# Performance work log

Hardware: AMD Instinct MI355X
Metric: run time of the kernel (lower is better)

## Reference

```python
import jax, jax.numpy as jnp
import numpy as np

B, S, D = 4, 2048, 1024
H = 16
DH = D // H          # 64
DFF = 4096
EPS = 1e-5


def _layer_norm(x, gamma, beta):
    mu = jnp.mean(x, axis=-1, keepdims=True)
    var = jnp.mean(jnp.square(x - mu), axis=-1, keepdims=True)
    return (x - mu) * jax.lax.rsqrt(var + EPS) * gamma + beta


def setup_inputs() -> dict:
    key = jax.random.key(0)
    ks = jax.random.split(key, 8)
    s_in = 1.0 / np.sqrt(D)
    s_ff = 1.0 / np.sqrt(DFF)
    return {
        "x": jax.random.normal(ks[0], (B, S, D), dtype=jnp.float32),
        # per-head qkv weights stacked: [H, D, 3*DH] (nn.Linear, bias=False)
        "Wqkv": jax.random.normal(ks[1], (H, D, 3 * DH), dtype=jnp.float32) * s_in,
        "Wproj": jax.random.normal(ks[2], (D, D), dtype=jnp.float32) * s_in,
        "bproj": jnp.zeros((D,), dtype=jnp.float32),
        "ln1_g": jnp.ones((D,), dtype=jnp.float32),
        "ln1_b": jnp.zeros((D,), dtype=jnp.float32),
        "ln2_g": jnp.ones((D,), dtype=jnp.float32),
        "ln2_b": jnp.zeros((D,), dtype=jnp.float32),
        "W1": jax.random.normal(ks[3], (D, DFF), dtype=jnp.float32) * s_in,
        "b1": jnp.zeros((DFF,), dtype=jnp.float32),
        "W2": jax.random.normal(ks[4], (DFF, D), dtype=jnp.float32) * s_ff,
        "b2": jnp.zeros((D,), dtype=jnp.float32),
    }


def reference(x, Wqkv, Wproj, bproj, ln1_g, ln1_b, ln2_g, ln2_b, W1, b1, W2, b2):
    # fused multi-head QKV projection: [B,S,D] x [H,D,3*DH] -> [B,H,S,3*DH]
    qkv = jnp.einsum('bsd,hde->bhse', x, Wqkv)
    q, k, v = jnp.split(qkv, 3, axis=-1)          # each [B,H,S,DH]
    scale = 1.0 / jnp.sqrt(jnp.asarray(DH, dtype=x.dtype))
    scores = jnp.einsum('bhsd,bhtd->bhst', q, k) * scale   # [B,H,S,S]
    causal = jnp.tril(jnp.ones((S, S), dtype=bool))
    scores = jnp.where(causal, scores, jnp.finfo(x.dtype).min)
    attn = jax.nn.softmax(scores, axis=-1)
    heads = jnp.einsum('bhst,bhtd->bhsd', attn, v)          # [B,H,S,DH]
    att_out = heads.transpose(0, 2, 1, 3).reshape(B, S, D)  # concat heads
    att_out = att_out @ Wproj + bproj
    out = _layer_norm(x + att_out, ln1_g, ln1_b)            # dropout = identity (eval)
    mlp_out = (jax.nn.gelu(out @ W1 + b1, approximate=False)) @ W2 + b2
    out = _layer_norm(out + mlp_out, ln2_g, ln2_b)
    return out
```

## Files before the change

### kernel.cpp

```cpp
#include <hip/hip_runtime.h>
#include <math.h>

#define BB 4
#define SS 2048
#define DD 1024
#define HH 16
#define DHH 64
#define DFF 4096
static constexpr float LN_EPS = 1e-5f;

typedef __bf16 bf16x8 __attribute__((ext_vector_type(8)));
typedef float f32x4 __attribute__((ext_vector_type(4)));
typedef unsigned short u16x8 __attribute__((ext_vector_type(8)));

__device__ __forceinline__ unsigned short f2bf(float f) {
    return __builtin_bit_cast(unsigned short, (__bf16)f);
}

__device__ __forceinline__ float fexp2(float x) {
    return __builtin_amdgcn_exp2f(x);
}

__device__ __forceinline__ void gl_lds16(const unsigned short* g,
                                         unsigned short* l) {
    __builtin_amdgcn_global_load_lds(
        (const __attribute__((address_space(1))) unsigned int*)g,
        (__attribute__((address_space(3))) unsigned int*)l, 16, 0, 0);
}

#define GBAR()                               \
    do {                                     \
        asm volatile("" ::: "memory");       \
        __builtin_amdgcn_s_barrier();        \
        asm volatile("" ::: "memory");       \
    } while (0)
#define VMCNT(n) asm volatile("s_waitcnt vmcnt(" #n ")" ::: "memory")

__global__ __launch_bounds__(256) void transpose_bf16_kernel(
    const float* __restrict__ in, unsigned short* __restrict__ outT,
    int R, int C) {
    __shared__ float t[64][65];
    const int r0 = blockIdx.y * 64, c0 = blockIdx.x * 64;
    const int cl = threadIdx.x & 63, rl = threadIdx.x >> 6;
#pragma unroll
    for (int rr = 0; rr < 16; ++rr)
        t[rl + rr * 4][cl] = in[(size_t)(r0 + rl + rr * 4) * C + c0 + cl];
    __syncthreads();
#pragma unroll
    for (int rr = 0; rr < 16; ++rr)
        outT[(size_t)(c0 + rl + rr * 4) * R + r0 + cl] = f2bf(t[cl][rl + rr * 4]);
}

__global__ __launch_bounds__(256) void repack_wqkv_bf16_kernel(
    const float* __restrict__ Wqkv, unsigned short* __restrict__ Wq2T) {
    __shared__ float t[64][65];
    const int h = blockIdx.z;
    const int d0 = blockIdx.y * 64, e0 = blockIdx.x * 64;
    const int cl = threadIdx.x & 63, rl = threadIdx.x >> 6;
#pragma unroll
    for (int rr = 0; rr < 16; ++rr)
        t[rl + rr * 4][cl] =
            Wqkv[((size_t)h * DD + d0 + rl + rr * 4) * 192 + e0 + cl];
    __syncthreads();
#pragma unroll
    for (int rr = 0; rr < 16; ++rr)
        Wq2T[((size_t)h * 192 + e0 + rl + rr * 4) * DD + d0 + cl] =
            f2bf(t[cl][rl + rr * 4]);
}

__global__ __launch_bounds__(256) void f2bf_kernel(
    const float* __restrict__ in, unsigned short* __restrict__ out, int n) {
    int i = blockIdx.x * 256 + threadIdx.x;
    if (i < n) out[i] = f2bf(in[i]);
}

template <int RS>
__device__ __forceinline__ void stage_half(const unsigned short* __restrict__ G,
                                           int ldK, int growbase, int kbase,
                                           unsigned short* lbase, int tid) {
#pragma unroll
    for (int s = 0; s < 2; ++s) {
        const int c16 = s * 512 + tid;
        const int r = c16 >> 3, c = c16 & 7;
        const int grow =
            growbase + ((r >> RS) << (RS + 1)) + (r & ((1 << RS) - 1));
        const int gcol = kbase + ((c ^ (r & 7)) << 3);
        gl_lds16(&G[(size_t)grow * ldK + gcol], &lbase[c16 << 3]);
    }
}

__device__ __forceinline__ void stage_64(const unsigned short* __restrict__ G,
                                         int ldK, int growbase, int kbase,
                                         unsigned short* lbase, int tid) {
    const int r = tid >> 3, c = tid & 7;
    const int grow = growbase + ((r >> 5) << 6) + (r & 31);
    const int gcol = kbase + ((c ^ (r & 7)) << 3);
    gl_lds16(&G[(size_t)grow * ldK + gcol], &lbase[tid << 3]);
}

__device__ __forceinline__ void stage_kv8(const unsigned short* __restrict__ src,
                                          size_t rstride, unsigned short* dst,
                                          int tid) {
    const int r = tid >> 3, c = tid & 7;
    gl_lds16(&src[(size_t)r * rstride + ((c ^ (r & 7)) << 3)], &dst[tid << 3]);
}

__device__ __forceinline__ void read_afrag(const unsigned short* s, int base,
                                           int wm, int l15, int g,
                                           bf16x8 af[4][2]) {
#pragma unroll
    for (int ii = 0; ii < 4; ++ii) {
        const int lr = wm * 64 + ii * 16 + l15;
#pragma unroll
        for (int ks = 0; ks < 2; ++ks) {
            const int p = ((ks << 2) + g) ^ (lr & 7);
            af[ii][ks] = __builtin_bit_cast(
                bf16x8, *(const u16x8*)&s[base + lr * 64 + p * 8]);
        }
    }
}

__device__ __forceinline__ void read_bfrag(const unsigned short* s, int base,
                                           int wn, int l15, int g,
                                           bf16x8 bf2[2][2]) {
#pragma unroll
    for (int jj = 0; jj < 2; ++jj) {
        const int lr = wn * 32 + jj * 16 + l15;
#pragma unroll
        for (int ks = 0; ks < 2; ++ks) {
            const int p = ((ks << 2) + g) ^ (lr & 7);
            bf2[jj][ks] = __builtin_bit_cast(
                bf16x8, *(const u16x8*)&s[base + lr * 64 + p * 8]);
        }
    }
}

template <int MH, int NH>
__device__ __forceinline__ void mfma_quad(f32x4 acc[8][4],
                                          const bf16x8 af[4][2],
                                          const bf16x8 bf2[2][2]) {
    __builtin_amdgcn_s_setprio(1);
#pragma unroll
    for (int ks = 0; ks < 2; ++ks)
#pragma unroll
        for (int ii = 0; ii < 4; ++ii)
#pragma unroll
            for (int jj = 0; jj < 2; ++jj)
                acc[MH * 4 + ii][NH * 2 + jj] =
                    __builtin_amdgcn_mfma_f32_16x16x32_bf16(
                        af[ii][ks], bf2[jj][ks],
                        acc[MH * 4 + ii][NH * 2 + jj], 0, 0, 0);
    __builtin_amdgcn_s_setprio(0);
}

template <int MODE>
__global__ __launch_bounds__(512) void mfma_gemm256_kernel(
    const unsigned short* __restrict__ A, const unsigned short* __restrict__ BT,
    float* __restrict__ Cf, unsigned short* __restrict__ Cb,
    const float* __restrict__ bias, const float* __restrict__ resid,
    int M, int N, int K) {
    __shared__ __align__(16) unsigned short smem[65536];
    const int tid = threadIdx.x;
    const int lane = tid & 63, wave = tid >> 6;
    const int wm = wave >> 2, wn = wave & 3;
    const int l15 = lane & 15, g = lane >> 4;

    const int gx = gridDim.x, nwg = gx * gridDim.y;
    const int lid = blockIdx.y * gx + blockIdx.x;
    const int swz = ((nwg & 7) == 0) ? ((lid & 7) * (nwg >> 3) + (lid >> 3))
                                     : lid;
    const int row0 = (swz / gx) * 256;
    const int col0 = (swz % gx) * 256;

    const int kt = K >> 6;

    f32x4 acc[8][4] = {};

    stage_half<6>(A, K, row0, 0, smem + 0, tid);
    stage_half<6>(A, K, row0 + 64, 0, smem + 8192, tid);
    stage_half<5>(BT, K, col0, 0, smem + 32768, tid);
    stage_half<5>(BT, K, col0 + 32, 0, smem + 40960, tid);
    VMCNT(4);
    stage_half<6>(A, K, row0, 64, smem + 16384, tid);
    stage_half<6>(A, K, row0 + 64, 64, smem + 24576, tid);
    stage_half<5>(BT, K, col0, 64, smem + 49152, tid);
    VMCNT(6);
    GBAR();

    bf16x8 af[4][2], bf0[2][2], bf1[2][2];
    for (int it = 0; it < (kt >> 1); ++it) {
        const int t1k = (2 * it + 1) << 6;
        int t2 = 2 * it + 2; if (t2 > kt - 1) t2 = kt - 1;
        int t3 = 2 * it + 3; if (t3 > kt - 1) t3 = kt - 1;
        const int t2k = t2 << 6, t3k = t3 << 6;

        read_afrag(smem, 0, wm, l15, g, af);
        read_bfrag(smem, 32768, wn, l15, g, bf0);
        stage_half<5>(BT, K, col0 + 32, t1k, smem + 57344, tid);
        GBAR();
        mfma_quad<0, 0>(acc, af, bf0);
        GBAR();

        read_bfrag(smem, 40960, wn, l15, g, bf1);
        stage_half<6>(A, K, row0, t2k, smem + 0, tid);
        GBAR();
        mfma_quad<0, 1>(acc, af, bf1);
        GBAR();

        read_afrag(smem, 8192, wm, l15, g, af);
        stage_half<5>(BT, K, col0, t2k, smem + 32768, tid);
        GBAR();
        mfma_quad<1, 1>(acc, af, bf1);
        GBAR();

        stage_half<6>(A, K, row0 + 64, t2k, smem + 8192, tid);
        GBAR();
        mfma_quad<1, 0>(acc, af, bf0);
        VMCNT(6);
        GBAR();

        read_afrag(smem, 16384, wm, l15, g, af);
        read_bfrag(smem, 49152, wn, l15, g, bf0);
        stage_half<5>(BT, K, col0 + 32, t2k, smem + 40960, tid);
        GBAR();
        mfma_quad<0, 0>(acc, af, bf0);
        GBAR();

        read_bfrag(smem, 57344, wn, l15, g, bf1);
        stage_half<6>(A, K, row0, t3k, smem + 16384, tid);
        GBAR();
        mfma_quad<0, 1>(acc, af, bf1);
        GBAR();

        read_afrag(smem, 24576, wm, l15, g, af);
        stage_half<5>(BT, K, col0, t3k, smem + 49152, tid);
        GBAR();
        mfma_quad<1, 1>(acc, af, bf1);
        GBAR();

        stage_half<6>(A, K, row0 + 64, t3k, smem + 24576, tid);
        GBAR();
        mfma_quad<1, 0>(acc, af, bf0);
        VMCNT(6);
        GBAR();
    }
    VMCNT(0);
    GBAR();

    if (MODE == 2) {
        constexpr int SLAB = 264;
#pragma unroll
        for (int i2 = 0; i2 < 8; ++i2) {
            __syncthreads();
#pragma unroll
            for (int j2 = 0; j2 < 4; ++j2) {
                const int col = wn * 64 + j2 * 16 + l15;
                const float bv = bias[col0 + col];
#pragma unroll
                for (int r = 0; r < 4; ++r) {
                    float v = acc[i2][j2][r] + bv;
                    float t = fexp2(v * (2.30211849f + 0.10294198f * v * v));
                    float gel = v * t * __builtin_amdgcn_rcpf(t + 1.f);
                    smem[(wm * 16 + g * 4 + r) * SLAB + col] = f2bf(gel);
                }
            }
            __syncthreads();
            const int sr = tid >> 4;
            const int cc = (tid & 15) * 16;
            const int grow = row0 + ((sr >> 4) << 7) + i2 * 16 + (sr & 15);
            *(u16x8*)&Cb[(size_t)grow * N + col0 + cc] =
                *(const u16x8*)&smem[sr * SLAB + cc];
            *(u16x8*)&Cb[(size_t)grow * N + col0 + cc + 8] =
                *(const u16x8*)&smem[sr * SLAB + cc + 8];
        }
        return;
    }

#pragma unroll
    for (int i2 = 0; i2 < 8; ++i2) {
#pragma unroll
        for (int j2 = 0; j2 < 4; ++j2) {
            const int col = col0 + wn * 64 + j2 * 16 + l15;
            const int rowb = row0 + wm * 128 + i2 * 16 + g * 4;
            const float bv = bias[col];
#pragma unroll
            for (int r = 0; r < 4; ++r) {
                const int row = rowb + r;
                float v = acc[i2][j2][r] + bv + resid[(size_t)row * N + col];
                Cf[(size_t)row * N + col] = v;
            }
        }
    }
}

__device__ __forceinline__ void read_af128(const unsigned short* s, int base,
                                           int wm, int l15, int g,
                                           bf16x8 af[2][2]) {
#pragma unroll
    for (int ii = 0; ii < 2; ++ii) {
        const int lr = wm * 32 + ii * 16 + l15;
#pragma unroll
        for (int ks = 0; ks < 2; ++ks) {
            const int p = ((ks << 2) + g) ^ (lr & 7);
            af[ii][ks] = __builtin_bit_cast(
                bf16x8, *(const u16x8*)&s[base + lr * 64 + p * 8]);
        }
    }
}

__device__ __forceinline__ void read_bf128(const unsigned short* s, int base,
                                           int wn, int l15, int g,
                                           bf16x8 bf2[2][2]) {
#pragma unroll
    for (int jj = 0; jj < 2; ++jj) {
        const int lr = wn * 32 + jj * 16 + l15;
#pragma unroll
        for (int ks = 0; ks < 2; ++ks) {
            const int p = ((ks << 2) + g) ^ (lr & 7);
            bf2[jj][ks] = __builtin_bit_cast(
                bf16x8, *(const u16x8*)&s[base + lr * 64 + p * 8]);
        }
    }
}

template <int MH, int NH>
__device__ __forceinline__ void mfma_quad128(f32x4 acc[4][4],
                                             const bf16x8 af[2][2],
                                             const bf16x8 bf2[2][2]) {
    __builtin_amdgcn_s_setprio(1);
#pragma unroll
    for (int ks = 0; ks < 2; ++ks)
#pragma unroll
        for (int ii = 0; ii < 2; ++ii)
#pragma unroll
            for (int jj = 0; jj < 2; ++jj)
                acc[MH * 2 + ii][NH * 2 + jj] =
                    __builtin_amdgcn_mfma_f32_16x16x32_bf16(
                        af[ii][ks], bf2[jj][ks],
                        acc[MH * 2 + ii][NH * 2 + jj], 0, 0, 0);
    __builtin_amdgcn_s_setprio(0);
}

template <int MODE>
__global__ __launch_bounds__(512) void gemm_n128_kernel(
    const unsigned short* __restrict__ A, const unsigned short* __restrict__ BT,
    float* __restrict__ Cf, const float* __restrict__ bias,
    const float* __restrict__ resid, unsigned short* __restrict__ Qb,
    unsigned short* __restrict__ Kb, unsigned short* __restrict__ VTb,
    int M, int N, int K) {
    __shared__ __align__(16) unsigned short smem[49152];
    const int tid = threadIdx.x;
    const int lane = tid & 63, wave = tid >> 6;
    const int wm = wave >> 1, wn = wave & 1;
    const int l15 = lane & 15, g = lane >> 4;

    const int gx = gridDim.x, nwg = gx * gridDim.y;
    const int lid = blockIdx.y * gx + blockIdx.x;
    const int swz = ((nwg & 7) == 0) ? ((lid & 7) * (nwg >> 3) + (lid >> 3))
                                     : lid;
    const int row0 = (swz / gx) * 256;
    const int col0 = (swz % gx) * 128;

    const int kt = K >> 6;

    f32x4 acc[4][4] = {};

    stage_half<5>(A, K, row0, 0, smem + 0, tid);
    stage_half<5>(A, K, row0 + 32, 0, smem + 8192, tid);
    stage_64(BT, K, col0, 0, smem + 32768, tid);
    stage_64(BT, K, col0 + 32, 0, smem + 36864, tid);
    VMCNT(4);
    stage_half<5>(A, K, row0, 64, smem + 16384, tid);
    stage_half<5>(A, K, row0 + 32, 64, smem + 24576, tid);
    stage_64(BT, K, col0, 64, smem + 40960, tid);
    VMCNT(5);
    GBAR();

    bf16x8 af[2][2], bf0[2][2], bf1[2][2];
    for (int it = 0; it < (kt >> 1); ++it) {
        const int t1k = (2 * it + 1) << 6;
        int t2 = 2 * it + 2; if (t2 > kt - 1) t2 = kt - 1;
        int t3 = 2 * it + 3; if (t3 > kt - 1) t3 = kt - 1;
        const int t2k = t2 << 6, t3k = t3 << 6;

        read_af128(smem, 0, wm, l15, g, af);
        read_bf128(smem, 32768, wn, l15, g, bf0);
        stage_64(BT, K, col0 + 32, t1k, smem + 45056, tid);
        GBAR();
        mfma_quad128<0, 0>(acc, af, bf0);
        GBAR();

        read_bf128(smem, 36864, wn, l15, g, bf1);
        stage_half<5>(A, K, row0, t2k, smem + 0, tid);
        GBAR();
        mfma_quad128<0, 1>(acc, af, bf1);
        GBAR();

        read_af128(smem, 8192, wm, l15, g, af);
        stage_64(BT, K, col0, t2k, smem + 32768, tid);
        GBAR();
        mfma_quad128<1, 1>(acc, af, bf1);
        GBAR();

        stage_half<5>(A, K, row0 + 32, t2k, smem + 8192, tid);
        GBAR();
        mfma_quad128<1, 0>(acc, af, bf0);
        VMCNT(5);
        GBAR();

        read_af128(smem, 16384, wm, l15, g, af);
        read_bf128(smem, 40960, wn, l15, g, bf0);
        stage_64(BT, K, col0 + 32, t2k, smem + 36864, tid);
        GBAR();
        mfma_quad128<0, 0>(acc, af, bf0);
        GBAR();

        read_bf128(smem, 45056, wn, l15, g, bf1);
        stage_half<5>(A, K, row0, t3k, smem + 16384, tid);
        GBAR();
        mfma_quad128<0, 1>(acc, af, bf1);
        GBAR();

        read_af128(smem, 24576, wm, l15, g, af);
        stage_64(BT, K, col0, t3k, smem + 40960, tid);
        GBAR();
        mfma_quad128<1, 1>(acc, af, bf1);
        GBAR();

        stage_half<5>(A, K, row0 + 32, t3k, smem + 24576, tid);
        GBAR();
        mfma_quad128<1, 0>(acc, af, bf0);
        VMCNT(5);
        GBAR();
    }
    VMCNT(0);
    GBAR();

#pragma unroll
    for (int i2 = 0; i2 < 4; ++i2) {
#pragma unroll
        for (int j2 = 0; j2 < 4; ++j2) {
            const int col = col0 + wn * 64 + j2 * 16 + l15;
            const int rowb = row0 + wm * 64 + i2 * 16 + g * 4;
            if (MODE == 4) {
                const int h = col / 192, e = col % 192;
                const int bb = rowb >> 11, s = rowb & 2047;
                if (e < 64) {
                    unsigned short* q =
                        Qb + (((size_t)bb * HH + h) * SS + s) * 64 + e;
#pragma unroll
                    for (int r = 0; r < 4; ++r)
                        q[r * 64] = f2bf(acc[i2][j2][r] * 0.18033688f);
                } else if (e < 128) {
                    unsigned short* kp =
                        Kb + (((size_t)bb * HH + h) * SS + s) * 64 + (e - 64);
#pragma unroll
                    for (int r = 0; r < 4; ++r)
                        kp[r * 64] = f2bf(acc[i2][j2][r]);
                } else {
                    ushort4 pk;
                    pk.x = f2bf(acc[i2][j2][0]);
                    pk.y = f2bf(acc[i2][j2][1]);
                    pk.z = f2bf(acc[i2][j2][2]);
                    pk.w = f2bf(acc[i2][j2][3]);
                    *(ushort4*)(VTb + (((size_t)bb * HH + h) * 64 + (e - 128)) *
                                          SS + s) = pk;
                }
            } else {
                const float bv = bias[col];
#pragma unroll
                for (int r = 0; r < 4; ++r) {
                    const int row = rowb + r;
                    float v = acc[i2][j2][r] + bv + resid[(size_t)row * N + col];
                    Cf[(size_t)row * N + col] = v;
                }
            }
        }
    }
}

__global__ __launch_bounds__(512) void fattn_kernel(
    const unsigned short* __restrict__ Qb, const unsigned short* __restrict__ Kb,
    const unsigned short* __restrict__ VTb, unsigned short* __restrict__ att) {
    constexpr int PSTR = 68;
    __shared__ __align__(16) unsigned short Pls[256 * PSTR];
    __shared__ __align__(16) unsigned short Kls[2][64 * 64];
    __shared__ __align__(16) unsigned short VTls[2][64 * 64];

    const int bh = blockIdx.x;
    const int p = blockIdx.y;
    const int qb = (p < 4) ? (7 - p) : (p - 4);
    const int q0 = qb * 256;
    const int tid = threadIdx.x;
    const int lane = tid & 63;
    const int wave = tid >> 6;
    const int l15 = lane & 15;
    const int g = lane >> 4;
    const int b = bh >> 4, h = bh & 15;

    const unsigned short* Qh = Qb + (size_t)bh * SS * 64;
    const unsigned short* Kh = Kb + (size_t)bh * SS * 64;
    const unsigned short* Vh = VTb + (size_t)bh * 64 * SS;

    {
        const int row = tid >> 1, c0 = (tid & 1) * 32;
        const unsigned short* src = Qh + (size_t)(q0 + row) * 64 + c0;
        unsigned short* dst = &Pls[row * PSTR + c0];
#pragma unroll
        for (int c = 0; c < 32; c += 8)
            *(u16x8*)(dst + c) = *(const u16x8*)(src + c);
    }
    bf16x8 qf[2][2];
#pragma unroll
    for (int i = 0; i < 2; ++i)
#pragma unroll
        for (int ks = 0; ks < 2; ++ks)
            qf[i][ks] = __builtin_bit_cast(
                bf16x8, *(const u16x8*)&Pls[(wave * 32 + i * 16 + l15) * PSTR +
                                            ks * 32 + g * 8]);

    f32x4 oacc[4][2] = {};
    float mst[2], lst[2];
#pragma unroll
    for (int i = 0; i < 2; ++i) { mst[i] = -1e30f; lst[i] = 0.f; }

    const int qlim = q0 + wave * 32 + 31;
    const int qrow = wave * 32 + l15;
    const int nt = qb * 4 + 4;
    const int xh = l15 & 7;

    stage_kv8(Kh, 64, &Kls[0][0], tid);
    stage_kv8(Vh, SS, &VTls[0][0], tid);

    for (int t = 0; t < nt; ++t) {
        const int t0 = t << 6;
        const int tn = (t + 1 < nt) ? t + 1 : nt - 1;
        stage_kv8(Kh + (size_t)(tn << 6) * 64, 64, &Kls[(t + 1) & 1][0], tid);
        stage_kv8(Vh + (tn << 6), SS, &VTls[(t + 1) & 1][0], tid);
        VMCNT(2);
        GBAR();

        if (t0 <= qlim) {
            const unsigned short* Kt = &Kls[t & 1][0];
            const unsigned short* Vt = &VTls[t & 1][0];

            f32x4 sacc[4][2] = {};
#pragma unroll
            for (int ks = 0; ks < 2; ++ks) {
                const int ko = ((((ks << 2) + g) ^ xh) << 3);
                bf16x8 kb[4];
#pragma unroll
                for (int j = 0; j < 4; ++j)
                    kb[j] = __builtin_bit_cast(
                        bf16x8, *(const u16x8*)&Kt[(j * 16 + l15) * 64 + ko]);
#pragma unroll
                for (int j = 0; j < 4; ++j)
#pragma unroll
                    for (int i = 0; i < 2; ++i)
                        sacc[j][i] = __builtin_amdgcn_mfma_f32_16x16x32_bf16(
                            kb[j], qf[i][ks], sacc[j][i], 0, 0, 0);
            }

            if (t0 + 63 > q0 + wave * 32) {
#pragma unroll
                for (int j = 0; j < 4; ++j)
#pragma unroll
                    for (int i = 0; i < 2; ++i)
#pragma unroll
                        for (int r = 0; r < 4; ++r) {
                            const int kg = t0 + j * 16 + g * 4 + r;
                            const int qg = q0 + qrow + i * 16;
                            if (kg > qg) sacc[j][i][r] = -1e30f;
                        }
            }

#pragma unroll
            for (int i = 0; i < 2; ++i) {
                float mx = -1e30f;
#pragma unroll
                for (int j = 0; j < 4; ++j)
                    mx = fmaxf(mx,
                               fmaxf(fmaxf(sacc[j][i][0], sacc[j][i][1]),
                                     fmaxf(sacc[j][i][2], sacc[j][i][3])));
                mx = fmaxf(mx, __shfl_xor(mx, 16));
                mx = fmaxf(mx, __shfl_xor(mx, 32));
                const bool grow = !__all(mx <= mst[i]);
                float al = 1.f;
                if (grow) {
                    const float mn = fmaxf(mst[i], mx);
                    al = fexp2(mst[i] - mn);
                    mst[i] = mn;
                }
                const float mm = mst[i];
                float rsum = 0.f;
                const int pbase = (qrow + i * 16) * PSTR + g * 4;
#pragma unroll
                for (int j = 0; j < 4; ++j) {
                    float p0 = fexp2(sacc[j][i][0] - mm);
                    float p1 = fexp2(sacc[j][i][1] - mm);
                    float p2 = fexp2(sacc[j][i][2] - mm);
                    float p3 = fexp2(sacc[j][i][3] - mm);
                    rsum += (p0 + p1) + (p2 + p3);
                    ushort4 pk;
                    pk.x = f2bf(p0); pk.y = f2bf(p1);
                    pk.z = f2bf(p2); pk.w = f2bf(p3);
                    *(ushort4*)&Pls[pbase + j * 16] = pk;
                }
                rsum += __shfl_xor(rsum, 16);
                rsum += __shfl_xor(rsum, 32);
                if (grow) {
                    lst[i] = lst[i] * al + rsum;
#pragma unroll
                    for (int jo = 0; jo < 4; ++jo)
#pragma unroll
                        for (int r = 0; r < 4; ++r) oacc[jo][i][r] *= al;
                } else {
                    lst[i] += rsum;
                }
            }

#pragma unroll
            for (int ks = 0; ks < 2; ++ks) {
                const int ko = ((((ks << 2) + g) ^ xh) << 3);
                bf16x8 vb[4], pf[2];
#pragma unroll
                for (int jo = 0; jo < 4; ++jo)
                    vb[jo] = __builtin_bit_cast(
                        bf16x8, *(const u16x8*)&Vt[(jo * 16 + l15) * 64 + ko]);
#pragma unroll
                for (int i = 0; i < 2; ++i)
                    pf[i] = __builtin_bit_cast(
                        bf16x8, *(const u16x8*)&Pls[(qrow + i * 16) * PSTR +
                                                    ks * 32 + g * 8]);
#pragma unroll
                for (int jo = 0; jo < 4; ++jo)
#pragma unroll
                    for (int i = 0; i < 2; ++i)
                        oacc[jo][i] = __builtin_amdgcn_mfma_f32_16x16x32_bf16(
                            vb[jo], pf[i], oacc[jo][i], 0, 0, 0);
            }
        }
        GBAR();
    }
    VMCNT(0);

#pragma unroll
    for (int i = 0; i < 2; ++i) {
        const float inv = 1.f / lst[i];
        const int qg = q0 + qrow + i * 16;
        unsigned short* dst = att + ((size_t)b * SS + qg) * DD + h * 64 + g * 4;
#pragma unroll
        for (int jo = 0; jo < 4; ++jo) {
            ushort4 pk;
            pk.x = f2bf(oacc[jo][i][0] * inv);
            pk.y = f2bf(oacc[jo][i][1] * inv);
            pk.z = f2bf(oacc[jo][i][2] * inv);
            pk.w = f2bf(oacc[jo][i][3] * inv);
            *(ushort4*)(dst + jo * 16) = pk;
        }
    }
}

__global__ __launch_bounds__(256) void ln_kernel(
    const float* __restrict__ X, const float* __restrict__ g,
    const float* __restrict__ bta, float* __restrict__ Y,
    unsigned short* __restrict__ Yb) {
    const int row = blockIdx.x;
    const float4 xv = ((const float4*)(X + (size_t)row * DD))[threadIdx.x];

    __shared__ float red1[4], red2[4];
    float s = xv.x + xv.y + xv.z + xv.w;
#pragma unroll
    for (int off = 32; off > 0; off >>= 1) s += __shfl_down(s, off);
    const int wave = threadIdx.x >> 6;
    if ((threadIdx.x & 63) == 0) red1[wave] = s;
    __syncthreads();
    const float mu = (red1[0] + red1[1] + red1[2] + red1[3]) * (1.f / DD);

    float dx = xv.x - mu, dy = xv.y - mu, dz = xv.z - mu, dw = xv.w - mu;
    float s2 = dx * dx + dy * dy + dz * dz + dw * dw;
#pragma unroll
    for (int off = 32; off > 0; off >>= 1) s2 += __shfl_down(s2, off);
    if ((threadIdx.x & 63) == 0) red2[wave] = s2;
    __syncthreads();
    const float var = (red2[0] + red2[1] + red2[2] + red2[3]) * (1.f / DD);
    const float rstd = rsqrtf(var + LN_EPS);

    const float4 gv = ((const float4*)g)[threadIdx.x];
    const float4 bv = ((const float4*)bta)[threadIdx.x];
    float4 yv;
    yv.x = dx * rstd * gv.x + bv.x;
    yv.y = dy * rstd * gv.y + bv.y;
    yv.z = dz * rstd * gv.z + bv.z;
    yv.w = dw * rstd * gv.w + bv.w;
    ((float4*)(Y + (size_t)row * DD))[threadIdx.x] = yv;
    if (Yb) {
        ushort4 q;
        q.x = f2bf(yv.x); q.y = f2bf(yv.y);
        q.z = f2bf(yv.z); q.w = f2bf(yv.w);
        ((ushort4*)(Yb + (size_t)row * DD))[threadIdx.x] = q;
    }
}

extern "C" void kernel_launch(void* const* d_in, const int* in_sizes, int n_in,
                              void* d_out, int out_size, void* d_ws,
                              size_t ws_size, hipStream_t stream) {
    const float* x     = (const float*)d_in[0];
    const float* Wqkv  = (const float*)d_in[1];
    const float* Wproj = (const float*)d_in[2];
    const float* bproj = (const float*)d_in[3];
    const float* ln1_g = (const float*)d_in[4];
    const float* ln1_b = (const float*)d_in[5];
    const float* ln2_g = (const float*)d_in[6];
    const float* ln2_b = (const float*)d_in[7];
    const float* W1    = (const float*)d_in[8];
    const float* b1    = (const float*)d_in[9];
    const float* W2    = (const float*)d_in[10];
    const float* b2    = (const float*)d_in[11];
    float* out = (float*)d_out;

    const size_t M = (size_t)BB * SS;
    const size_t MB = 1024 * 1024;
    char* w = (char*)d_ws;
    unsigned short* Qb     = (unsigned short*)(w + 0);
    unsigned short* out1b  = (unsigned short*)(w + 0);
    unsigned short* Kb     = (unsigned short*)(w + 16 * MB);
    unsigned short* VTb    = (unsigned short*)(w + 32 * MB);
    unsigned short* hbuf   = (unsigned short*)(w + 16 * MB);
    unsigned short* Wq2T   = (unsigned short*)(w + 96 * MB);
    unsigned short* xb     = (unsigned short*)(w + 102 * MB);
    unsigned short* att    = (unsigned short*)(w + 96 * MB);
    float*          out1   = (float*)(w + 96 * MB);
    unsigned short* WprojT = (unsigned short*)(w + 118 * MB);
    unsigned short* W1T    = (unsigned short*)(w + 128 * MB);
    unsigned short* W2T    = (unsigned short*)(w + 136 * MB);

    repack_wqkv_bf16_kernel<<<dim3(3, 16, 16), 256, 0, stream>>>(Wqkv, Wq2T);
    transpose_bf16_kernel<<<dim3(16, 16), 256, 0, stream>>>(Wproj, WprojT, 1024, 1024);
    transpose_bf16_kernel<<<dim3(64, 16), 256, 0, stream>>>(W1, W1T, 1024, 4096);
    transpose_bf16_kernel<<<dim3(16, 64), 256, 0, stream>>>(W2, W2T, 4096, 1024);
    f2bf_kernel<<<(int)((M * DD + 255) / 256), 256, 0, stream>>>(x, xb, (int)(M * DD));

    gemm_n128_kernel<4><<<dim3(3072 / 128, M / 256), 512, 0, stream>>>(
        xb, Wq2T, nullptr, nullptr, nullptr, Qb, Kb, VTb, (int)M, 3072, 1024);

    fattn_kernel<<<dim3(BB * HH, SS / 256), 512, 0, stream>>>(Qb, Kb, VTb, att);

    gemm_n128_kernel<3><<<dim3(1024 / 128, M / 256), 512, 0, stream>>>(
        att, WprojT, out, bproj, x, nullptr, nullptr, nullptr,
        (int)M, 1024, 1024);

    ln_kernel<<<(int)M, 256, 0, stream>>>(out, ln1_g, ln1_b, out1, out1b);

    mfma_gemm256_kernel<2><<<dim3(4096 / 256, M / 256), 512, 0, stream>>>(
        out1b, W1T, nullptr, hbuf, b1, nullptr, (int)M, 4096, 1024);

    gemm_n128_kernel<3><<<dim3(1024 / 128, M / 256), 512, 0, stream>>>(
        hbuf, W2T, out, b2, out1, nullptr, nullptr, nullptr,
        (int)M, 1024, 4096);

    ln_kernel<<<(int)M, 256, 0, stream>>>(out, ln2_g, ln2_b, out, nullptr);
}
```

Baseline: 497.1 us.

## Restructure flash attention into paired 128-row causal chunks with register-shuffled P

Each block now handles two 128-query chunks, p and 15-p, one after the other so causal work is balanced across blocks. Each wave owns 16 query rows instead of 32. The softmax probabilities are rearranged into the MFMA B-operand layout with cross-lane shuffles instead of a round trip through LDS, and the P/Q LDS buffer is removed. MFMA sections get raised scheduling priority and launch bounds request more resident blocks. The trade-off is that K/V tiles are staged again for the second chunk, and each K/V tile now feeds half as many query rows.

```diff
diff --git a/kernel.cpp b/kernel.cpp
--- a/kernel.cpp
+++ b/kernel.cpp
@@ -12,6 +12,7 @@
 typedef __bf16 bf16x8 __attribute__((ext_vector_type(8)));
 typedef float f32x4 __attribute__((ext_vector_type(4)));
 typedef unsigned short u16x8 __attribute__((ext_vector_type(8)));
+typedef unsigned int u32x4 __attribute__((ext_vector_type(4)));
 
 __device__ __forceinline__ unsigned short f2bf(float f) {
     return __builtin_bit_cast(unsigned short, (__bf16)f);
@@ -479,185 +480,183 @@
     }
 }
 
-__global__ __launch_bounds__(512) void fattn_kernel(
+__global__ __launch_bounds__(512, 4) void fattn_kernel(
     const unsigned short* __restrict__ Qb, const unsigned short* __restrict__ Kb,
     const unsigned short* __restrict__ VTb, unsigned short* __restrict__ att) {
-    constexpr int PSTR = 68;
-    __shared__ __align__(16) unsigned short Pls[256 * PSTR];
     __shared__ __align__(16) unsigned short Kls[2][64 * 64];
     __shared__ __align__(16) unsigned short VTls[2][64 * 64];
 
     const int bh = blockIdx.x;
     const int p = blockIdx.y;
-    const int qb = (p < 4) ? (7 - p) : (p - 4);
-    const int q0 = qb * 256;
     const int tid = threadIdx.x;
     const int lane = tid & 63;
     const int wave = tid >> 6;
     const int l15 = lane & 15;
     const int g = lane >> 4;
     const int b = bh >> 4, h = bh & 15;
+    const int xh = l15 & 7;
 
     const unsigned short* Qh = Qb + (size_t)bh * SS * 64;
     const unsigned short* Kh = Kb + (size_t)bh * SS * 64;
     const unsigned short* Vh = VTb + (size_t)bh * 64 * SS;
 
-    {
-        const int row = tid >> 1, c0 = (tid & 1) * 32;
-        const unsigned short* src = Qh + (size_t)(q0 + row) * 64 + c0;
-        unsigned short* dst = &Pls[row * PSTR + c0];
-#pragma unroll
-        for (int c = 0; c < 32; c += 8)
-            *(u16x8*)(dst + c) = *(const u16x8*)(src + c);
-    }
-    bf16x8 qf[2][2];
-#pragma unroll
-    for (int i = 0; i < 2; ++i)
+    const int srcA = l15 | ((lane & 16) << 1);
+    const int srcB = srcA | 16;
+    const bool ghi = (lane & 32) != 0;
+
+#pragma unroll 1
+    for (int half = 0; half < 2; ++half) {
+        const int cidx = half ? (15 - p) : p;
+        const int q0c = cidx << 7;
+        const int qrow = wave * 16 + l15;
+        const int qg = q0c + qrow;
+        const int qlim = q0c + wave * 16 + 15;
+        const int nt = (cidx << 1) + 2;
+
+        bf16x8 qf[2];
 #pragma unroll
         for (int ks = 0; ks < 2; ++ks)
-            qf[i][ks] = __builtin_bit_cast(
-                bf16x8, *(const u16x8*)&Pls[(wave * 32 + i * 16 + l15) * PSTR +
-                                            ks * 32 + g * 8]);
-
-    f32x4 oacc[4][2] = {};
-    float mst[2], lst[2];
-#pragma unroll
-    for (int i = 0; i < 2; ++i) { mst[i] = -1e30f; lst[i] = 0.f; }
-
-    const int qlim = q0 + wave * 32 + 31;
-    const int qrow = wave * 32 + l15;
-    const int nt = qb * 4 + 4;
-    const int xh = l15 & 7;
-
-    stage_kv8(Kh, 64, &Kls[0][0], tid);
-    stage_kv8(Vh, SS, &VTls[0][0], tid);
-
-    for (int t = 0; t < nt; ++t) {
-        const int t0 = t << 6;
-        const int tn = (t + 1 < nt) ? t + 1 : nt - 1;
-        stage_kv8(Kh + (size_t)(tn << 6) * 64, 64, &Kls[(t + 1) & 1][0], tid);
-        stage_kv8(Vh + (tn << 6), SS, &VTls[(t + 1) & 1][0], tid);
-        VMCNT(2);
-        GBAR();
-
-        if (t0 <= qlim) {
-            const unsigned short* Kt = &Kls[t & 1][0];
-            const unsigned short* Vt = &VTls[t & 1][0];
-
-            f32x4 sacc[4][2] = {};
-#pragma unroll
-            for (int ks = 0; ks < 2; ++ks) {
-                const int ko = ((((ks << 2) + g) ^ xh) << 3);
-                bf16x8 kb[4];
-#pragma unroll
-                for (int j = 0; j < 4; ++j)
-                    kb[j] = __builtin_bit_cast(
-                        bf16x8, *(const u16x8*)&Kt[(j * 16 + l15) * 64 + ko]);
-#pragma unroll
-                for (int j = 0; j < 4; ++j)
-#pragma unroll
-                    for (int i = 0; i < 2; ++i)
-                        sacc[j][i] = __builtin_amdgcn_mfma_f32_16x16x32_bf16(
-                            kb[j], qf[i][ks], sacc[j][i], 0, 0, 0);
+            qf[ks] = __builtin_bit_cast(
+                bf16x8, *(const u16x8*)&Qh[(size_t)qg * 64 + ks * 32 + g * 8]);
+
+        f32x4 oacc[4] = {};
+        float mst = -1e30f, lst = 0.f;
+
+        stage_kv8(Kh, 64, &Kls[0][0], tid);
+        stage_kv8(Vh, SS, &VTls[0][0], tid);
+
+        for (int t = 0; t < nt; ++t) {
+            const int t0 = t << 6;
+            if (t + 1 < nt) {
+                stage_kv8(Kh + ((size_t)(t + 1) << 6) * 64, 64,
+                          &Kls[(t + 1) & 1][0], tid);
+                stage_kv8(Vh + ((t + 1) << 6), SS, &VTls[(t + 1) & 1][0], tid);
+                VMCNT(2);
+            } else {
+                VMCNT(0);
             }
-
-            if (t0 + 63 > q0 + wave * 32) {
-#pragma unroll
-                for (int j = 0; j < 4; ++j)
-#pragma unroll
-                    for (int i = 0; i < 2; ++i)
+            GBAR();
+
+            if (t0 <= qlim) {
+                const unsigned short* Kt = &Kls[t & 1][0];
+                const unsigned short* Vt = &VTls[t & 1][0];
+
+                f32x4 sacc[4] = {};
+                __builtin_amdgcn_s_setprio(1);
+#pragma unroll
+                for (int ks = 0; ks < 2; ++ks) {
+                    const int ko = ((((ks << 2) + g) ^ xh) << 3);
+                    bf16x8 kb[4];
+#pragma unroll
+                    for (int j = 0; j < 4; ++j)
+                        kb[j] = __builtin_bit_cast(
+                            bf16x8,
+                            *(const u16x8*)&Kt[(j * 16 + l15) * 64 + ko]);
+#pragma unroll
+                    for (int j = 0; j < 4; ++j)
+                        sacc[j] = __builtin_amdgcn_mfma_f32_16x16x32_bf16(
+                            kb[j], qf[ks], sacc[j], 0, 0, 0);
+                }
+                __builtin_amdgcn_s_setprio(0);
+
+                if (t0 + 63 > q0c + wave * 16) {
+#pragma unroll
+                    for (int j = 0; j < 4; ++j)
 #pragma unroll
                         for (int r = 0; r < 4; ++r) {
                             const int kg = t0 + j * 16 + g * 4 + r;
-                            const int qg = q0 + qrow + i * 16;
-                            if (kg > qg) sacc[j][i][r] = -1e30f;
+                            if (kg > qg) sacc[j][r] = -1e30f;
                         }
-            }
-
-#pragma unroll
-            for (int i = 0; i < 2; ++i) {
+                }
+
                 float mx = -1e30f;
 #pragma unroll
                 for (int j = 0; j < 4; ++j)
-                    mx = fmaxf(mx,
-                               fmaxf(fmaxf(sacc[j][i][0], sacc[j][i][1]),
-                                     fmaxf(sacc[j][i][2], sacc[j][i][3])));
+                    mx = fmaxf(mx, fmaxf(fmaxf(sacc[j][0], sacc[j][1]),
+                                         fmaxf(sacc[j][2], sacc[j][3])));
                 mx = fmaxf(mx, __shfl_xor(mx, 16));
                 mx = fmaxf(mx, __shfl_xor(mx, 32));
-                const bool grow = !__all(mx <= mst[i]);
+                const bool grow = !__all(mx <= mst);
                 float al = 1.f;
                 if (grow) {
-                    const float mn = fmaxf(mst[i], mx);
-                    al = fexp2(mst[i] - mn);
-                    mst[i] = mn;
-                }
-                const float mm = mst[i];
+                    const float mn = fmaxf(mst, mx);
+                    al = fexp2(mst - mn);
+                    mst = mn;
+                }
+                const float mm = mst;
                 float rsum = 0.f;
-                const int pbase = (qrow + i * 16) * PSTR + g * 4;
+                unsigned int Aw[4], Bw[4];
 #pragma unroll
                 for (int j = 0; j < 4; ++j) {
-                    float p0 = fexp2(sacc[j][i][0] - mm);
-                    float p1 = fexp2(sacc[j][i][1] - mm);
-                    float p2 = fexp2(sacc[j][i][2] - mm);
-                    float p3 = fexp2(sacc[j][i][3] - mm);
+                    float p0 = fexp2(sacc[j][0] - mm);
+                    float p1 = fexp2(sacc[j][1] - mm);
+                    float p2 = fexp2(sacc[j][2] - mm);
+                    float p3 = fexp2(sacc[j][3] - mm);
                     rsum += (p0 + p1) + (p2 + p3);
-                    ushort4 pk;
-                    pk.x = f2bf(p0); pk.y = f2bf(p1);
-                    pk.z = f2bf(p2); pk.w = f2bf(p3);
-                    *(ushort4*)&Pls[pbase + j * 16] = pk;
+                    Aw[j] = (unsigned int)f2bf(p0) |
+                            ((unsigned int)f2bf(p1) << 16);
+                    Bw[j] = (unsigned int)f2bf(p2) |
+                            ((unsigned int)f2bf(p3) << 16);
                 }
                 rsum += __shfl_xor(rsum, 16);
                 rsum += __shfl_xor(rsum, 32);
                 if (grow) {
-                    lst[i] = lst[i] * al + rsum;
+                    lst = lst * al + rsum;
 #pragma unroll
                     for (int jo = 0; jo < 4; ++jo)
 #pragma unroll
-                        for (int r = 0; r < 4; ++r) oacc[jo][i][r] *= al;
+                        for (int r = 0; r < 4; ++r) oacc[jo][r] *= al;
                 } else {
-                    lst[i] += rsum;
+                    lst += rsum;
+                }
+
+#pragma unroll
+                for (int ks = 0; ks < 2; ++ks) {
+                    const int jl = ks * 2, jh = ks * 2 + 1;
+                    const int aLo0 = __shfl((int)Aw[jl], srcA);
+                    const int aHi0 = __shfl((int)Aw[jh], srcA);
+                    const int bLo0 = __shfl((int)Bw[jl], srcA);
+                    const int bHi0 = __shfl((int)Bw[jh], srcA);
+                    const int aLo1 = __shfl((int)Aw[jl], srcB);
+                    const int aHi1 = __shfl((int)Aw[jh], srcB);
+                    const int bLo1 = __shfl((int)Bw[jl], srcB);
+                    const int bHi1 = __shfl((int)Bw[jh], srcB);
+                    u32x4 pw;
+                    pw[0] = (unsigned int)(ghi ? aHi0 : aLo0);
+                    pw[1] = (unsigned int)(ghi ? bHi0 : bLo0);
+                    pw[2] = (unsigned int)(ghi ? aHi1 : aLo1);
+                    pw[3] = (unsigned int)(ghi ? bHi1 : bLo1);
+                    const bf16x8 pf = __builtin_bit_cast(bf16x8, pw);
+
+                    const int ko = ((((ks << 2) + g) ^ xh) << 3);
+                    __builtin_amdgcn_s_setprio(1);
+#pragma unroll
+                    for (int jo = 0; jo < 4; ++jo) {
+                        const bf16x8 vb = __builtin_bit_cast(
+                            bf16x8,
+                            *(const u16x8*)&Vt[(jo * 16 + l15) * 64 + ko]);
+                        oacc[jo] = __builtin_amdgcn_mfma_f32_16x16x32_bf16(
+                            vb, pf, oacc[jo], 0, 0, 0);
+                    }
+                    __builtin_amdgcn_s_setprio(0);
                 }
             }
-
-#pragma unroll
-            for (int ks = 0; ks < 2; ++ks) {
-                const int ko = ((((ks << 2) + g) ^ xh) << 3);
-                bf16x8 vb[4], pf[2];
-#pragma unroll
-                for (int jo = 0; jo < 4; ++jo)
-                    vb[jo] = __builtin_bit_cast(
-                        bf16x8, *(const u16x8*)&Vt[(jo * 16 + l15) * 64 + ko]);
-#pragma unroll
-                for (int i = 0; i < 2; ++i)
-                    pf[i] = __builtin_bit_cast(
-                        bf16x8, *(const u16x8*)&Pls[(qrow + i * 16) * PSTR +
-                                                    ks * 32 + g * 8]);
-#pragma unroll
-                for (int jo = 0; jo < 4; ++jo)
-#pragma unroll
-                    for (int i = 0; i < 2; ++i)
-                        oacc[jo][i] = __builtin_amdgcn_mfma_f32_16x16x32_bf16(
-                            vb[jo], pf[i], oacc[jo][i], 0, 0, 0);
-            }
-        }
-        GBAR();
-    }
-    VMCNT(0);
-
-#pragma unroll
-    for (int i = 0; i < 2; ++i) {
-        const float inv = 1.f / lst[i];
-        const int qg = q0 + qrow + i * 16;
-        unsigned short* dst = att + ((size_t)b * SS + qg) * DD + h * 64 + g * 4;
+            GBAR();
+        }
+
+        const float inv = 1.f / lst;
+        unsigned short* dst =
+            att + ((size_t)b * SS + qg) * DD + h * 64 + g * 4;
 #pragma unroll
         for (int jo = 0; jo < 4; ++jo) {
             ushort4 pk;
-            pk.x = f2bf(oacc[jo][i][0] * inv);
-            pk.y = f2bf(oacc[jo][i][1] * inv);
-            pk.z = f2bf(oacc[jo][i][2] * inv);
-            pk.w = f2bf(oacc[jo][i][3] * inv);
+            pk.x = f2bf(oacc[jo][0] * inv);
+            pk.y = f2bf(oacc[jo][1] * inv);
+            pk.z = f2bf(oacc[jo][2] * inv);
+            pk.w = f2bf(oacc[jo][3] * inv);
             *(ushort4*)(dst + jo * 16) = pk;
         }
+        GBAR();
     }
 }
 
@@ -744,7 +743,7 @@
     gemm_n128_kernel<4><<<dim3(3072 / 128, M / 256), 512, 0, stream>>>(
         xb, Wq2T, nullptr, nullptr, nullptr, Qb, Kb, VTb, (int)M, 3072, 1024);
 
-    fattn_kernel<<<dim3(BB * HH, SS / 256), 512, 0, stream>>>(Qb, Kb, VTb, att);
+    fattn_kernel<<<dim3(BB * HH, 8), 512, 0, stream>>>(Qb, Kb, VTb, att);
 
     gemm_n128_kernel<3><<<dim3(1024 / 128, M / 256), 512, 0, stream>>>(
         att, WprojT, out, bproj, x, nullptr, nullptr, nullptr,
```

Result: faster. 483.9 us (-2.6%).
